# Kernel tuning notes

Hardware: AMD Instinct MI355X
Metric: run time of the kernel (lower is better)

Reference implementation:

```python
import jax, jax.numpy as jnp
import numpy as np

N, E, D, EF, C, G, NPG = 50000, 500000, 16, 8, 10, 500, 100
NUM_LAYERS = 3
EPS = 1e-5


def setup_inputs() -> dict:
    key = jax.random.key(0)
    ks = jax.random.split(key, 16)
    s = 0.1
    return {
        'x': jax.random.normal(ks[0], (N, D), jnp.float32),
        'edge_attr': jax.random.normal(ks[1], (E, EF), jnp.float32),
        # edge MLP (shared across all NNConv layers, as in the source)
        'edge_w1': jax.random.normal(ks[2], (EF, D), jnp.float32) * s,
        'edge_b1': jnp.zeros((D,), jnp.float32),
        'edge_w2': jax.random.normal(ks[3], (D, D * D), jnp.float32) * s,
        'edge_b2': jnp.zeros((D * D,), jnp.float32),
        # per-layer NNConv root weight + bias
        'root': jax.random.normal(ks[4], (NUM_LAYERS, D, D), jnp.float32) * s,
        'conv_bias': jnp.zeros((NUM_LAYERS, D), jnp.float32),
        # per-layer BatchNorm affine params
        'bn_gamma': jnp.ones((NUM_LAYERS, D), jnp.float32),
        'bn_beta': jnp.zeros((NUM_LAYERS, D), jnp.float32),
        # readout MLP
        'fc1_w': jax.random.normal(ks[5], (4 * D, D), jnp.float32) * s,
        'fc1_b': jnp.zeros((D,), jnp.float32),
        'fc2_w': jax.random.normal(ks[6], (D, C), jnp.float32) * s,
        'fc2_b': jnp.zeros((C,), jnp.float32),
        # graph structure (constants w.r.t. grads)
        'edge_index': jax.random.randint(ks[7], (2, E), 0, N, dtype=jnp.int32),
        'lengths': jnp.full((G,), NPG, dtype=jnp.int32),
    }


def reference(x, edge_attr, edge_w1, edge_b1, edge_w2, edge_b2, root,
              conv_bias, bn_gamma, bn_beta, fc1_w, fc1_b, fc2_w, fc2_b,
              edge_index, lengths):
    src, dst = edge_index[0], edge_index[1]
    # Edge MLP -> per-edge weight matrices [E, D, D] (edge_attr is layer-invariant,
    # so the shared edge_model output is computed once).
    h_e = jnp.tanh(edge_attr @ edge_w1 + edge_b1)
    W = (h_e @ edge_w2 + edge_b2).reshape(E, D, D)
    # in-degree for mean aggregation (nodes with no incoming edges -> 0)
    deg = jax.ops.segment_sum(jnp.ones((E,), x.dtype), dst, num_segments=N)
    deg = jnp.maximum(deg, 1.0)[:, None]

    h = x
    for l in range(NUM_LAYERS):
        # NNConv: gather -> per-edge matvec -> scatter-mean, plus root term + bias
        msg = jnp.einsum('ei,eio->eo', h[src], W)          # [E, D]
        agg = jax.ops.segment_sum(msg, dst, num_segments=N) / deg
        h = agg + h @ root[l] + conv_bias[l]
        # BatchNorm over nodes (training-mode batch statistics, biased var)
        mu = h.mean(axis=0)
        var = h.var(axis=0)
        h = (h - mu) * jax.lax.rsqrt(var + EPS) * bn_gamma[l] + bn_beta[l]
        h = jnp.tanh(h)  # Dropout is identity in eval mode

    hidden = h
    # ragged segment pooling: graph id per node from lengths
    seg = jnp.repeat(jnp.arange(G), lengths, total_repeat_length=N)
    sum_p = jax.ops.segment_sum(hidden, seg, num_segments=G)
    cnt = jnp.maximum(lengths.astype(hidden.dtype), 1)[:, None]
    mean_p = sum_p / cnt
    max_p = jax.ops.segment_max(hidden, seg, num_segments=G)
    min_p = jax.ops.segment_min(hidden, seg, num_segments=G)
    pooled = jnp.concatenate([mean_p, max_p, min_p, sum_p], axis=1)  # [G, 4D]

    fc = jnp.tanh(pooled @ fc1_w + fc1_b)
    fc = fc @ fc2_w + fc2_b
    out = jax.nn.log_softmax(fc, axis=1)
    return hidden, pooled, fc, out
```

## Files before the change

### kernel.cpp

```cpp
#include <hip/hip_runtime.h>

#define D 16
#define EFD 8
#define NREP 64
#define TSTRIDE 272


__global__ void k_zero2(int* a, int na, float* b, int nb) {
    int i = blockIdx.x * 256 + threadIdx.x;
    if (i < na) a[i] = 0;
    if (i < nb) b[i] = 0.f;
}


__global__ void k_rank2(const int* __restrict__ src, const int* __restrict__ dst,
                        int* __restrict__ cntS, int* __restrict__ cntD,
                        int* __restrict__ rankS, int* __restrict__ rankD, int E_) {
    int e = blockIdx.x * 256 + threadIdx.x;
    if (e < E_) {
        rankS[e] = atomicAdd(&cntS[src[e]], 1);
        rankD[e] = atomicAdd(&cntD[dst[e]], 1);
    }
}


__global__ void k_scanA2(const int* __restrict__ cnt2, int* __restrict__ offs2,
                         int* __restrict__ bsum2, int n, int nScan) {
    __shared__ int s[1024];
    int half = blockIdx.x / nScan;
    int blk  = blockIdx.x % nScan;
    const int* c = cnt2 + (size_t)half * n;
    int* of = offs2 + (size_t)half * (n + 1);
    int* bs = bsum2 + half * 64;
    int i = blk * 1024 + threadIdx.x;
    int v = (i < n) ? c[i] : 0;
    s[threadIdx.x] = v;
    __syncthreads();
    for (int d = 1; d < 1024; d <<= 1) {
        int t = (threadIdx.x >= d) ? s[threadIdx.x - d] : 0;
        __syncthreads();
        s[threadIdx.x] += t;
        __syncthreads();
    }
    int incl = s[threadIdx.x];
    if (i < n) of[i] = incl - v;
    if (threadIdx.x == 1023) bs[blk] = incl;
}

__global__ void k_scanC2(int* __restrict__ offs2, const int* __restrict__ bsum2,
                         int n, int nScan, int total) {
    __shared__ int s[64];
    int half = blockIdx.x / nScan;
    int blk  = blockIdx.x % nScan;
    int* of = offs2 + (size_t)half * (n + 1);
    const int* bs = bsum2 + half * 64;
    if (threadIdx.x < 64) s[threadIdx.x] = (threadIdx.x < nScan) ? bs[threadIdx.x] : 0;
    __syncthreads();
    if (threadIdx.x < 64) {
        for (int d = 1; d < 64; d <<= 1) {
            int t = (threadIdx.x >= d) ? s[threadIdx.x - d] : 0;
            __syncthreads();
            s[threadIdx.x] += t;
            __syncthreads();
        }
    } else {
        for (int d = 1; d < 64; d <<= 1) { __syncthreads(); __syncthreads(); }
    }
    int base = (blk == 0) ? 0 : s[blk - 1];
    int i = blk * 1024 + threadIdx.x;
    if (i < n) of[i] += base;
    else if (i == n) of[n] = total;
}


__global__ void k_place_he(const int* __restrict__ src, const int* __restrict__ dst,
                           const int* __restrict__ rankS, const int* __restrict__ rankD,
                           const int* __restrict__ offsS, const int* __restrict__ offsD,
                           const float* __restrict__ ea, const float* __restrict__ w1,
                           const float* __restrict__ b1,
                           float* __restrict__ hE, int* __restrict__ permInv, int E_) {
    __shared__ float w1s[EFD * D];
    __shared__ float b1s[D];
    if (threadIdx.x < EFD * D) w1s[threadIdx.x] = w1[threadIdx.x];
    if (threadIdx.x < D) b1s[threadIdx.x] = b1[threadIdx.x];
    __syncthreads();
    int e = blockIdx.x * 256 + threadIdx.x;
    if (e >= E_) return;
    int p = offsS[src[e]] + rankS[e];
    int q = offsD[dst[e]] + rankD[e];
    permInv[p] = q;
    const float4* a4 = (const float4*)(ea + (size_t)e * EFD);
    float4 x0 = a4[0], x1 = a4[1];
    float out[D];
#pragma unroll
    for (int o = 0; o < D; o++) {
        float s = b1s[o];
        s += x0.x * w1s[0 * D + o] + x0.y * w1s[1 * D + o] +
             x0.z * w1s[2 * D + o] + x0.w * w1s[3 * D + o] +
             x1.x * w1s[4 * D + o] + x1.y * w1s[5 * D + o] +
             x1.z * w1s[6 * D + o] + x1.w * w1s[7 * D + o];
        out[o] = tanhf(s);
    }
    float4* h4 = (float4*)(hE + (size_t)p * D);
#pragma unroll
    for (int v = 0; v < 4; v++)
        h4[v] = make_float4(out[v * 4 + 0], out[v * 4 + 1], out[v * 4 + 2], out[v * 4 + 3]);
}


__global__ void k_Tmsg(const float* __restrict__ hin, const float* __restrict__ statsPrev,
                       const float* __restrict__ gamma, const float* __restrict__ beta,
                       float* __restrict__ hout, const float* __restrict__ w2,
                       const float* __restrict__ b2, const float* __restrict__ hE,
                       const int* __restrict__ offsS, const int* __restrict__ permInv,
                       float* __restrict__ msg, int n, int useBN) {
    __shared__ float hs[16 * D];
    __shared__ float Tt[16 * TSTRIDE];
    __shared__ float sstats[32];
    int tid = threadIdx.x;
    int j = tid >> 4, o = tid & 15;
    float w16[16], b16[16];
#pragma unroll
    for (int i = 0; i < 16; i++) w16[i] = w2[j * 256 + i * 16 + o];
#pragma unroll
    for (int i = 0; i < 16; i++) b16[i] = b2[i * 16 + o];
    if (useBN && tid < 32) {
        float a = 0.f;
#pragma unroll 8
        for (int r = 0; r < NREP; r++) a += statsPrev[r * 32 + tid];
        sstats[tid] = a;
    }
    __syncthreads();
    int base = blockIdx.x * 16;
    float fn = (float)n;
    {
        int node = base + j;
        float hv = 0.f;
        if (node < n) {
            float xin = hin[(size_t)node * D + o];
            if (useBN) {
                float mu = sstats[o] / fn;
                float var = sstats[16 + o] / fn - mu * mu;
                hv = tanhf((xin - mu) * rsqrtf(var + 1e-5f) * gamma[o] + beta[o]);
                hout[(size_t)node * D + o] = hv;
            } else {
                hv = xin;
            }
        }
        hs[tid] = hv;
    }
    __syncthreads();
    {
        const float4* hs4 = (const float4*)hs;
#pragma unroll
        for (int nb = 0; nb < 16; nb++) {
            float4 h0 = hs4[nb * 4 + 0], h1 = hs4[nb * 4 + 1];
            float4 h2 = hs4[nb * 4 + 2], h3 = hs4[nb * 4 + 3];
            float s = h0.x * w16[0]  + h0.y * w16[1]  + h0.z * w16[2]  + h0.w * w16[3]
                    + h1.x * w16[4]  + h1.y * w16[5]  + h1.z * w16[6]  + h1.w * w16[7]
                    + h2.x * w16[8]  + h2.y * w16[9]  + h2.z * w16[10] + h2.w * w16[11]
                    + h3.x * w16[12] + h3.y * w16[13] + h3.z * w16[14] + h3.w * w16[15];
            Tt[nb * TSTRIDE + tid] = s;
        }
        float4 h0 = hs4[j * 4 + 0], h1 = hs4[j * 4 + 1];
        float4 h2 = hs4[j * 4 + 2], h3 = hs4[j * 4 + 3];
        float s = h0.x * b16[0]  + h0.y * b16[1]  + h0.z * b16[2]  + h0.w * b16[3]
                + h1.x * b16[4]  + h1.y * b16[5]  + h1.z * b16[6]  + h1.w * b16[7]
                + h2.x * b16[8]  + h2.y * b16[9]  + h2.z * b16[10] + h2.w * b16[11]
                + h3.x * b16[12] + h3.y * b16[13] + h3.z * b16[14] + h3.w * b16[15];
        Tt[j * TSTRIDE + 256 + o] = s;
    }
    __syncthreads();
    {
        int slot = j;
        int s = base + slot;
        if (s >= n) return;
        float tr[D];
#pragma unroll
        for (int jj = 0; jj < D; jj++) tr[jj] = Tt[slot * TSTRIDE + jj * 16 + o];
        float tb = Tt[slot * TSTRIDE + 256 + o];
        int p0 = offsS[s], p1 = offsS[s + 1];
        for (int p = p0; p < p1; p++) {
            const float4* he4 = (const float4*)(hE + (size_t)p * D);
            float4 a0 = he4[0], a1 = he4[1], a2 = he4[2], a3 = he4[3];
            float a = tb
                + a0.x * tr[0]  + a0.y * tr[1]  + a0.z * tr[2]  + a0.w * tr[3]
                + a1.x * tr[4]  + a1.y * tr[5]  + a1.z * tr[6]  + a1.w * tr[7]
                + a2.x * tr[8]  + a2.y * tr[9]  + a2.z * tr[10] + a2.w * tr[11]
                + a3.x * tr[12] + a3.y * tr[13] + a3.z * tr[14] + a3.w * tr[15];
            int q = permInv[p];
            msg[(size_t)q * D + o] = a;
        }
    }
}


__global__ void k_agg(const float* __restrict__ h, const float* __restrict__ msg,
                      const int* __restrict__ offsD, const float* __restrict__ root_l,
                      const float* __restrict__ cbias, float* __restrict__ hpre,
                      float* __restrict__ statsR, int n) {
    __shared__ float rootS[D * D];
    __shared__ float red[256], red2[256];
    if (threadIdx.x < D * D) rootS[threadIdx.x] = root_l[threadIdx.x];
    __syncthreads();
    int slot = threadIdx.x >> 4, o = threadIdx.x & 15;
    int node = blockIdx.x * 16 + slot;
    float acc = 0.f;
    if (node < n) {
        int p0 = offsD[node], p1 = offsD[node + 1];
        float sum = 0.f;
        int p = p0;
        for (; p + 4 <= p1; p += 4) {
            float a0 = msg[(size_t)(p + 0) * D + o];
            float a1 = msg[(size_t)(p + 1) * D + o];
            float a2 = msg[(size_t)(p + 2) * D + o];
            float a3 = msg[(size_t)(p + 3) * D + o];
            sum += (a0 + a1) + (a2 + a3);
        }
        for (; p < p1; p++) sum += msg[(size_t)p * D + o];
        float deg = (float)((p1 - p0) > 1 ? (p1 - p0) : 1);
        float r = cbias[o];
        const float* hr = h + (size_t)node * D;
#pragma unroll
        for (int i = 0; i < D; i++) r += hr[i] * rootS[i * D + o];
        acc = sum / deg + r;
        hpre[(size_t)node * D + o] = acc;
    }
    red[threadIdx.x] = acc;
    red2[threadIdx.x] = acc * acc;
    __syncthreads();
    for (int off = 128; off >= 16; off >>= 1) {
        if (threadIdx.x < off) {
            red[threadIdx.x] += red[threadIdx.x + off];
            red2[threadIdx.x] += red2[threadIdx.x + off];
        }
        __syncthreads();
    }
    if (threadIdx.x < 32) {
        float v = (threadIdx.x < 16) ? red[threadIdx.x] : red2[threadIdx.x - 16];
        atomicAdd(&statsR[(blockIdx.x & (NREP - 1)) * 32 + threadIdx.x], v);
    }
}


__global__ void k_readout(const float* __restrict__ hpre, const float* __restrict__ statsR,
                          const float* __restrict__ gamma, const float* __restrict__ beta,
                          const int* __restrict__ lengths,
                          const float* __restrict__ w1, const float* __restrict__ b1,
                          const float* __restrict__ w2, const float* __restrict__ b2,
                          float* __restrict__ outHidden, float* __restrict__ outPooled,
                          float* __restrict__ fcOut, float* __restrict__ lsmOut,
                          int Gc, int n) {
    __shared__ int sl[512];
    __shared__ float sstats[32];
    int tid = threadIdx.x;
    int g = blockIdx.x;
    if (tid < 32) {
        float a = 0.f;
#pragma unroll 8
        for (int r = 0; r < NREP; r++) a += statsR[r * 32 + tid];
        sstats[tid] = a;
    }
    int v = (tid < Gc) ? lengths[tid] : 0;
    sl[tid] = v;
    __syncthreads();
    for (int d = 1; d < 512; d <<= 1) {
        int t = (tid >= d) ? sl[tid - d] : 0;
        __syncthreads();
        sl[tid] += t;
        __syncthreads();
    }
    int n1 = sl[g];
    int n0 = n1 - lengths[g];
    float fn = (float)n;
    int slot = tid >> 4, o = tid & 15;
    float mu = sstats[o] / fn;
    float var = sstats[16 + o] / fn - mu * mu;
    float rstd = rsqrtf(var + 1e-5f);
    float gm = gamma[o], bt = beta[o];
    float s = 0.f, mx = -3.402823466e38f, mn = 3.402823466e38f;
    for (int nd = n0 + slot; nd < n1; nd += 32) {
        float xin = hpre[(size_t)nd * D + o];
        float x = tanhf((xin - mu) * rstd * gm + bt);
        outHidden[(size_t)nd * D + o] = x;
        s += x;
        mx = fmaxf(mx, x);
        mn = fminf(mn, x);
    }
    __shared__ float rs[512], rmx[512], rmn[512];
    rs[tid] = s; rmx[tid] = mx; rmn[tid] = mn;
    __syncthreads();
    for (int off = 256; off >= 16; off >>= 1) {
        if (tid < off) {
            rs[tid] += rs[tid + off];
            rmx[tid] = fmaxf(rmx[tid], rmx[tid + off]);
            rmn[tid] = fminf(rmn[tid], rmn[tid + off]);
        }
        __syncthreads();
    }
    __shared__ float p64[64], t16[16], f10[10];
    __shared__ float mred, lred;
    if (tid < 16) {
        float cnt = fmaxf((float)(n1 - n0), 1.f);
        float sum = rs[tid];
        float* row = outPooled + (size_t)g * 64;
        float mean = sum / cnt;
        p64[tid] = mean;          row[tid] = mean;
        p64[16 + tid] = rmx[tid]; row[16 + tid] = rmx[tid];
        p64[32 + tid] = rmn[tid]; row[32 + tid] = rmn[tid];
        p64[48 + tid] = sum;      row[48 + tid] = sum;
    }
    __syncthreads();
    if (tid < 16) {
        float a = b1[tid];
        for (int k = 0; k < 64; k++) a += p64[k] * w1[k * 16 + tid];
        t16[tid] = tanhf(a);
    }
    __syncthreads();
    if (tid < 10) {
        float a = b2[tid];
        for (int oo = 0; oo < 16; oo++) a += t16[oo] * w2[oo * 10 + tid];
        f10[tid] = a;
        fcOut[(size_t)g * 10 + tid] = a;
    }
    __syncthreads();
    if (tid == 0) {
        float m = f10[0];
        for (int c = 1; c < 10; c++) m = fmaxf(m, f10[c]);
        float se = 0.f;
        for (int c = 0; c < 10; c++) se += expf(f10[c] - m);
        mred = m;
        lred = logf(se);
    }
    __syncthreads();
    if (tid < 10)
        lsmOut[(size_t)g * 10 + tid] = f10[tid] - mred - lred;
}


extern "C" void kernel_launch(void* const* d_in, const int* in_sizes, int n_in,
                              void* d_out, int out_size, void* d_ws, size_t ws_size,
                              hipStream_t stream) {
    const float* x    = (const float*)d_in[0];
    const float* ea   = (const float*)d_in[1];
    const float* ew1  = (const float*)d_in[2];
    const float* eb1  = (const float*)d_in[3];
    const float* ew2  = (const float*)d_in[4];
    const float* eb2  = (const float*)d_in[5];
    const float* root = (const float*)d_in[6];
    const float* cb   = (const float*)d_in[7];
    const float* gam  = (const float*)d_in[8];
    const float* bet  = (const float*)d_in[9];
    const float* f1w  = (const float*)d_in[10];
    const float* f1b  = (const float*)d_in[11];
    const float* f2w  = (const float*)d_in[12];
    const float* f2b  = (const float*)d_in[13];
    const int* eidx   = (const int*)d_in[14];
    const int* lens   = (const int*)d_in[15];

    int N  = in_sizes[0] / D;
    int E_ = in_sizes[1] / EFD;
    int Gc = in_sizes[15];
    const int* srcIdx = eidx;
    const int* dstIdx = eidx + E_;

    float* outHidden = (float*)d_out;
    float* outPooled = outHidden + (size_t)N * D;
    float* outFc     = outPooled + (size_t)Gc * 4 * D;
    float* outLsm    = outFc + (size_t)Gc * 10;

    char* wsp = (char*)d_ws;
    size_t off = 0;
    auto alloc = [&](size_t bytes) -> void* {
        void* p = wsp + off;
        off = (off + bytes + 255) & ~(size_t)255;
        return p;
    };
    int*   cnt2    = (int*)alloc((size_t)2 * N * 4);
    int*   offs2   = (int*)alloc((size_t)2 * (N + 1) * 4);
    int*   bsum2   = (int*)alloc(128 * 4);
    int*   rankS   = (int*)alloc((size_t)E_ * 4);
    int*   rankD   = (int*)alloc((size_t)E_ * 4);
    int*   permInv = (int*)alloc((size_t)E_ * 4);
    float* hE      = (float*)alloc((size_t)E_ * D * 4);
    float* msg     = (float*)alloc((size_t)E_ * D * 4);
    float* bufA    = (float*)alloc((size_t)N * D * 4);
    float* tmp     = (float*)alloc((size_t)N * D * 4);
    float* statsR3 = (float*)alloc((size_t)3 * NREP * 32 * 4);

    int* offsS = offs2;
    int* offsD = offs2 + (N + 1);
    int nScan = (N + 1023) / 1024;

    k_zero2<<<(2 * N + 255) / 256, 256, 0, stream>>>(cnt2, 2 * N, statsR3, 3 * NREP * 32);
    k_rank2<<<(E_ + 255) / 256, 256, 0, stream>>>(srcIdx, dstIdx, cnt2, cnt2 + N,
                                                  rankS, rankD, E_);
    k_scanA2<<<2 * nScan, 1024, 0, stream>>>(cnt2, offs2, bsum2, N, nScan);
    k_scanC2<<<2 * nScan, 1024, 0, stream>>>(offs2, bsum2, N, nScan, E_);
    k_place_he<<<(E_ + 255) / 256, 256, 0, stream>>>(srcIdx, dstIdx, rankS, rankD,
                                                     offsS, offsD, ea, ew1, eb1,
                                                     hE, permInv, E_);

    for (int l = 0; l < 3; l++) {
        const float* hin   = (l == 0) ? x : tmp;
        const float* hroot = (l == 0) ? x : bufA;
        float* statsCur = statsR3 + (size_t)l * NREP * 32;
        const float* statsPrev = statsR3 + (size_t)(l - 1) * NREP * 32;
        k_Tmsg<<<(N + 15) / 16, 256, 0, stream>>>(
            hin, (l == 0) ? nullptr : statsPrev,
            (l == 0) ? nullptr : gam + (size_t)(l - 1) * 16,
            (l == 0) ? nullptr : bet + (size_t)(l - 1) * 16,
            bufA, ew2, eb2, hE, offsS, permInv, msg, N, (l == 0) ? 0 : 1);
        k_agg<<<(N + 15) / 16, 256, 0, stream>>>(hroot, msg, offsD,
                                                 root + (size_t)l * 256, cb + (size_t)l * 16,
                                                 tmp, statsCur, N);
    }

    k_readout<<<Gc, 512, 0, stream>>>(tmp, statsR3 + (size_t)2 * NREP * 32,
                                      gam + 32, bet + 32, lens, f1w, f1b, f2w, f2b,
                                      outHidden, outPooled, outFc, outLsm, Gc, N);
}
```

Baseline: 332.4 us.

## Make k_Tmsg wave-local so each wavefront handles four nodes without block barriers

Restructures the per-node transform kernel so each 64-lane wavefront normalizes, stores and transforms its own four nodes. This removes the block-wide __syncthreads and the shared stats buffer: BN statistics are reduced per wave and broadcast with shuffles. Each thread now holds 64 w2 weights in registers and computes the bias term directly from global b2. The costs are higher register pressure and therefore possibly lower occupancy. It also relies on wave-synchronous LDS visibility without explicit barriers or fences.

```diff
diff --git a/kernel.cpp b/kernel.cpp
--- a/kernel.cpp
+++ b/kernel.cpp
@@ -116,81 +116,96 @@
                        float* __restrict__ msg, int n, int useBN) {
     __shared__ float hs[16 * D];
     __shared__ float Tt[16 * TSTRIDE];
-    __shared__ float sstats[32];
     int tid = threadIdx.x;
-    int j = tid >> 4, o = tid & 15;
-    float w16[16], b16[16];
-#pragma unroll
-    for (int i = 0; i < 16; i++) w16[i] = w2[j * 256 + i * 16 + o];
-#pragma unroll
-    for (int i = 0; i < 16; i++) b16[i] = b2[i * 16 + o];
-    if (useBN && tid < 32) {
+    int lane = tid & 63;
+    int w = tid >> 6;
+    int jj = lane >> 4;
+    int o = lane & 15;
+    int slotG = (w << 2) + jj;
+    int base = blockIdx.x * 16;
+    int node = base + slotG;
+    float fn = (float)n;
+
+    float mu = 0.f, rstd = 1.f, gm = 1.f, bt = 0.f;
+    if (useBN) {
         float a = 0.f;
+        int c = lane & 31;
 #pragma unroll 8
-        for (int r = 0; r < NREP; r++) a += statsPrev[r * 32 + tid];
-        sstats[tid] = a;
-    }
-    __syncthreads();
-    int base = blockIdx.x * 16;
-    float fn = (float)n;
-    {
-        int node = base + j;
-        float hv = 0.f;
-        if (node < n) {
-            float xin = hin[(size_t)node * D + o];
-            if (useBN) {
-                float mu = sstats[o] / fn;
-                float var = sstats[16 + o] / fn - mu * mu;
-                hv = tanhf((xin - mu) * rsqrtf(var + 1e-5f) * gamma[o] + beta[o]);
-                hout[(size_t)node * D + o] = hv;
-            } else {
-                hv = xin;
-            }
-        }
-        hs[tid] = hv;
-    }
-    __syncthreads();
-    {
-        const float4* hs4 = (const float4*)hs;
-#pragma unroll
-        for (int nb = 0; nb < 16; nb++) {
-            float4 h0 = hs4[nb * 4 + 0], h1 = hs4[nb * 4 + 1];
-            float4 h2 = hs4[nb * 4 + 2], h3 = hs4[nb * 4 + 3];
-            float s = h0.x * w16[0]  + h0.y * w16[1]  + h0.z * w16[2]  + h0.w * w16[3]
-                    + h1.x * w16[4]  + h1.y * w16[5]  + h1.z * w16[6]  + h1.w * w16[7]
-                    + h2.x * w16[8]  + h2.y * w16[9]  + h2.z * w16[10] + h2.w * w16[11]
-                    + h3.x * w16[12] + h3.y * w16[13] + h3.z * w16[14] + h3.w * w16[15];
-            Tt[nb * TSTRIDE + tid] = s;
-        }
-        float4 h0 = hs4[j * 4 + 0], h1 = hs4[j * 4 + 1];
-        float4 h2 = hs4[j * 4 + 2], h3 = hs4[j * 4 + 3];
-        float s = h0.x * b16[0]  + h0.y * b16[1]  + h0.z * b16[2]  + h0.w * b16[3]
-                + h1.x * b16[4]  + h1.y * b16[5]  + h1.z * b16[6]  + h1.w * b16[7]
-                + h2.x * b16[8]  + h2.y * b16[9]  + h2.z * b16[10] + h2.w * b16[11]
-                + h3.x * b16[12] + h3.y * b16[13] + h3.z * b16[14] + h3.w * b16[15];
-        Tt[j * TSTRIDE + 256 + o] = s;
-    }
-    __syncthreads();
-    {
-        int slot = j;
-        int s = base + slot;
-        if (s >= n) return;
-        float tr[D];
-#pragma unroll
-        for (int jj = 0; jj < D; jj++) tr[jj] = Tt[slot * TSTRIDE + jj * 16 + o];
-        float tb = Tt[slot * TSTRIDE + 256 + o];
-        int p0 = offsS[s], p1 = offsS[s + 1];
-        for (int p = p0; p < p1; p++) {
-            const float4* he4 = (const float4*)(hE + (size_t)p * D);
-            float4 a0 = he4[0], a1 = he4[1], a2 = he4[2], a3 = he4[3];
-            float a = tb
-                + a0.x * tr[0]  + a0.y * tr[1]  + a0.z * tr[2]  + a0.w * tr[3]
-                + a1.x * tr[4]  + a1.y * tr[5]  + a1.z * tr[6]  + a1.w * tr[7]
-                + a2.x * tr[8]  + a2.y * tr[9]  + a2.z * tr[10] + a2.w * tr[11]
-                + a3.x * tr[12] + a3.y * tr[13] + a3.z * tr[14] + a3.w * tr[15];
-            int q = permInv[p];
-            msg[(size_t)q * D + o] = a;
-        }
+        for (int r = 0; r < NREP; r++) a += statsPrev[r * 32 + c];
+        float sm = __shfl(a, o);
+        float s2 = __shfl(a, 16 + o);
+        mu = sm / fn;
+        float var = s2 / fn - mu * mu;
+        rstd = rsqrtf(var + 1e-5f);
+        gm = gamma[o]; bt = beta[o];
+    }
+    float hv = 0.f;
+    if (node < n) {
+        float xin = hin[(size_t)node * D + o];
+        if (useBN) {
+            hv = tanhf((xin - mu) * rstd * gm + bt);
+            hout[(size_t)node * D + o] = hv;
+        } else {
+            hv = xin;
+        }
+    }
+    hs[slotG * D + o] = hv;
+
+    float w16[4][16];
+#pragma unroll
+    for (int r = 0; r < 4; r++)
+#pragma unroll
+        for (int i = 0; i < 16; i++)
+            w16[r][i] = w2[(4 * jj + r) * 256 + i * 16 + o];
+
+    const float4* hs4 = (const float4*)hs;
+    float4 g0 = hs4[slotG * 4 + 0], g1 = hs4[slotG * 4 + 1];
+    float4 g2 = hs4[slotG * 4 + 2], g3 = hs4[slotG * 4 + 3];
+    float tb = g0.x * b2[0 * 16 + o]  + g0.y * b2[1 * 16 + o]
+             + g0.z * b2[2 * 16 + o]  + g0.w * b2[3 * 16 + o]
+             + g1.x * b2[4 * 16 + o]  + g1.y * b2[5 * 16 + o]
+             + g1.z * b2[6 * 16 + o]  + g1.w * b2[7 * 16 + o]
+             + g2.x * b2[8 * 16 + o]  + g2.y * b2[9 * 16 + o]
+             + g2.z * b2[10 * 16 + o] + g2.w * b2[11 * 16 + o]
+             + g3.x * b2[12 * 16 + o] + g3.y * b2[13 * 16 + o]
+             + g3.z * b2[14 * 16 + o] + g3.w * b2[15 * 16 + o];
+
+#pragma unroll
+    for (int nbl = 0; nbl < 4; nbl++) {
+        int nb = (w << 2) + nbl;
+        float4 h0 = hs4[nb * 4 + 0], h1 = hs4[nb * 4 + 1];
+        float4 h2 = hs4[nb * 4 + 2], h3 = hs4[nb * 4 + 3];
+#pragma unroll
+        for (int r = 0; r < 4; r++) {
+            float s = h0.x * w16[r][0]  + h0.y * w16[r][1]
+                    + h0.z * w16[r][2]  + h0.w * w16[r][3]
+                    + h1.x * w16[r][4]  + h1.y * w16[r][5]
+                    + h1.z * w16[r][6]  + h1.w * w16[r][7]
+                    + h2.x * w16[r][8]  + h2.y * w16[r][9]
+                    + h2.z * w16[r][10] + h2.w * w16[r][11]
+                    + h3.x * w16[r][12] + h3.y * w16[r][13]
+                    + h3.z * w16[r][14] + h3.w * w16[r][15];
+            Tt[nb * TSTRIDE + (4 * jj + r) * 16 + o] = s;
+        }
+    }
+
+    float tr[16];
+#pragma unroll
+    for (int j2 = 0; j2 < 16; j2++)
+        tr[j2] = Tt[slotG * TSTRIDE + j2 * 16 + o];
+
+    if (node >= n) return;
+    int p0 = offsS[node], p1 = offsS[node + 1];
+    for (int p = p0; p < p1; p++) {
+        const float4* he4 = (const float4*)(hE + (size_t)p * D);
+        float4 a0 = he4[0], a1 = he4[1], a2 = he4[2], a3 = he4[3];
+        float a = tb
+            + a0.x * tr[0]  + a0.y * tr[1]  + a0.z * tr[2]  + a0.w * tr[3]
+            + a1.x * tr[4]  + a1.y * tr[5]  + a1.z * tr[6]  + a1.w * tr[7]
+            + a2.x * tr[8]  + a2.y * tr[9]  + a2.z * tr[10] + a2.w * tr[11]
+            + a3.x * tr[12] + a3.y * tr[13] + a3.z * tr[14] + a3.w * tr[15];
+        int q = permInv[p];
+        msg[(size_t)q * D + o] = a;
     }
 }
 
```

After: 336.4 us. No clear change (+1.2%).
